# Performance work log

Measured on AMD Instinct MI355X. Metric: run time of the kernel, lower is better.

## Reference

```python
import jax, jax.numpy as jnp
import numpy as np

B, S_ENC, S_DEC = 4, 2048, 1024
ENC_DIM, DEC_DIM, H = 1024, 1024, 16
CROSS_DIM = max(ENC_DIM, DEC_DIM)
HEAD_DIM_DEC = DEC_DIM // H
SCALE = HEAD_DIM_DEC ** 0.5  # module divides by dec_scaling only


def _linear_params(key, d_in, d_out):
    kw, kb = jax.random.split(key)
    bound = 1.0 / np.sqrt(d_in)
    W = jax.random.uniform(kw, (d_in, d_out), jnp.float32, -bound, bound)
    b = jax.random.uniform(kb, (d_out,), jnp.float32, -bound, bound)
    return W, b


def setup_inputs() -> dict:
    key = jax.random.key(0)
    ks = jax.random.split(key, 7)
    enc = jax.random.normal(ks[0], (B, S_ENC, ENC_DIM), jnp.float32)
    dec = jax.random.normal(ks[1], (B, S_DEC, DEC_DIM), jnp.float32)
    enc_mask = jax.random.uniform(ks[2], (B, 1, 1, S_ENC)) < 0.1
    q_w, q_b = _linear_params(ks[3], DEC_DIM, CROSS_DIM)
    k_w, k_b = _linear_params(ks[4], ENC_DIM, CROSS_DIM)
    v_w, v_b = _linear_params(ks[5], ENC_DIM, DEC_DIM)
    o_w, o_b = _linear_params(ks[6], DEC_DIM, DEC_DIM)
    return {"enc": enc, "enc_mask": enc_mask, "dec": dec,
            "q_w": q_w, "q_b": q_b, "k_w": k_w, "k_b": k_b,
            "v_w": v_w, "v_b": v_b, "o_w": o_w, "o_b": o_b}


def _split_heads(x):
    b, s, d = x.shape
    return x.reshape(b, s, H, d // H).transpose(0, 2, 1, 3)  # [b,h,s,hd]


def reference(enc, enc_mask, dec, q_w, q_b, k_w, k_b, v_w, v_b, o_w, o_b):
    q = _split_heads(dec @ q_w + q_b)   # [B,H,Sq,cross_hd]
    k = _split_heads(enc @ k_w + k_b)   # [B,H,Sk,cross_hd]
    v = _split_heads(enc @ v_w + v_b)   # [B,H,Sk,dec_hd]
    logits = jnp.einsum('bhqd,bhkd->bhqk', q, k) / SCALE
    logits = jnp.where(enc_mask, -jnp.inf, logits)
    a = jax.nn.softmax(logits, axis=-1)
    x = jnp.einsum('bhqk,bhkd->bhqd', a, v)          # [B,H,Sq,dec_hd]
    x = x.transpose(0, 2, 1, 3).reshape(x.shape[0], x.shape[2], -1)  # [B,Sq,DEC_DIM]
    return x @ o_w + o_b
```

## Files before the change

kernel.cpp:

```cpp
#include <hip/hip_runtime.h>
#include <hip/hip_bf16.h>
#include <cstdint>

#define BB   4
#define SENC 2048
#define SDEC 1024
#define DM   1024
#define NH   16
#define HD   64

using short8 = __attribute__((ext_vector_type(8))) short;
using f32x4  = __attribute__((ext_vector_type(4))) float;

__device__ inline unsigned short f2bf(float f) {
    return (unsigned short)((__builtin_bit_cast(unsigned int, f) + 0x8000u) >> 16);
}
__device__ inline unsigned int pk2bf(float a, float b) {
    return ((__builtin_bit_cast(unsigned int, a) + 0x8000u) >> 16) |
           ((__builtin_bit_cast(unsigned int, b) + 0x8000u) & 0xffff0000u);
}

__device__ inline float fexp2(float x) {
#if __has_builtin(__builtin_amdgcn_exp2f)
    return __builtin_amdgcn_exp2f(x);
#else
    return exp2f(x);
#endif
}

#if __has_builtin(__builtin_amdgcn_global_load_lds)
#define HAS_GLL 1
#endif

__device__ inline void stage16(const void* g, void* l) {
#ifdef HAS_GLL
    typedef __attribute__((address_space(1))) const unsigned int guint;
    typedef __attribute__((address_space(3))) unsigned int luint;
    __builtin_amdgcn_global_load_lds((guint*)g, (luint*)l, 16, 0, 0);
#else
    *(short8*)l = *(const short8*)g;
#endif
}

__global__ __launch_bounds__(256) void prep_kernel(
    const float* __restrict__ dec, const float* __restrict__ enc,
    unsigned short* __restrict__ actb,
    const float* __restrict__ qw, const float* __restrict__ kw,
    const float* __restrict__ vw, const float* __restrict__ ow,
    unsigned short* __restrict__ qwt, unsigned short* __restrict__ kvwt,
    unsigned short* __restrict__ owt) {
    __shared__ float t[64][65];
    const int id = blockIdx.x, tid = threadIdx.x;
    if (id < 12288) {
        const int nd = BB * SDEC * DM;
        int i = (id * 256 + tid) * 4;
        const float* src = (i < nd) ? (dec + i) : (enc + (i - nd));
        float4 v = *(const float4*)src;
        ushort4 o;
        o.x = f2bf(v.x); o.y = f2bf(v.y); o.z = f2bf(v.z); o.w = f2bf(v.w);
        *(ushort4*)(actb + i) = o;
        return;
    }
    const int id2 = id - 12288;
    const int z = id2 >> 8, ky = (id2 >> 4) & 15, nx = id2 & 15;
    const float* src; unsigned short* dst;
    switch (z) {
        case 0:  src = qw; dst = qwt; break;
        case 1:  src = kw; dst = kvwt; break;
        case 2:  src = vw; dst = kvwt + (size_t)64 * 16384; break;
        default: src = ow; dst = owt; break;
    }
    const int k0 = ky * 64, n0 = nx * 64;
    #pragma unroll
    for (int it = 0; it < 16; ++it) {
        int e = it * 256 + tid, r = e >> 6, c = e & 63;
        t[r][c] = src[(size_t)(k0 + r) * DM + n0 + c];
    }
    __syncthreads();
    #pragma unroll
    for (int it = 0; it < 16; ++it) {
        int e = it * 256 + tid, r = e >> 6, c = e & 63;
        size_t off = (size_t)((n0 + r) >> 4) * 16384 + (size_t)((k0 + c) >> 3) * 128
                   + ((r & 15) << 3) + (c & 7);
        dst[off] = f2bf(t[c][r]);
    }
}

#define FENCE() asm volatile("" ::: "memory")
#define BARRIER() do { FENCE(); __builtin_amdgcn_s_barrier(); FENCE(); } while (0)

#define STAGE_TILE(kt, bufi) do { \
    stage16(Ab + (kt) * 64,          &As[bufi][tid * 8]); \
    stage16(Ab + 65536 + (kt) * 64,  &As[bufi][4096 + tid * 8]); \
    stage16(Ab + 131072 + (kt) * 64, &As[bufi][8192 + tid * 8]); \
    stage16(Ab + 196608 + (kt) * 64, &As[bufi][12288 + tid * 8]); \
} while (0)

#define LOADB(dst, kt) do { \
    dst[0][0] = *(const short8*)&Bbase[(kt) * 1024]; \
    dst[0][1] = *(const short8*)&Bbase[(kt) * 1024 + 512]; \
    dst[1][0] = *(const short8*)&Bbase[16384 + (kt) * 1024]; \
    dst[1][1] = *(const short8*)&Bbase[16384 + (kt) * 1024 + 512]; \
    dst[2][0] = *(const short8*)&Bbase[32768 + (kt) * 1024]; \
    dst[2][1] = *(const short8*)&Bbase[32768 + (kt) * 1024 + 512]; \
    dst[3][0] = *(const short8*)&Bbase[49152 + (kt) * 1024]; \
    dst[3][1] = *(const short8*)&Bbase[49152 + (kt) * 1024 + 512]; \
} while (0)

#define MFMA8(ii, a0, a1) do { \
    acc[ii][0] = __builtin_amdgcn_mfma_f32_16x16x32_bf16(a0, bcur[0][0], acc[ii][0], 0, 0, 0); \
    acc[ii][1] = __builtin_amdgcn_mfma_f32_16x16x32_bf16(a0, bcur[1][0], acc[ii][1], 0, 0, 0); \
    acc[ii][2] = __builtin_amdgcn_mfma_f32_16x16x32_bf16(a0, bcur[2][0], acc[ii][2], 0, 0, 0); \
    acc[ii][3] = __builtin_amdgcn_mfma_f32_16x16x32_bf16(a0, bcur[3][0], acc[ii][3], 0, 0, 0); \
    acc[ii][0] = __builtin_amdgcn_mfma_f32_16x16x32_bf16(a1, bcur[0][1], acc[ii][0], 0, 0, 0); \
    acc[ii][1] = __builtin_amdgcn_mfma_f32_16x16x32_bf16(a1, bcur[1][1], acc[ii][1], 0, 0, 0); \
    acc[ii][2] = __builtin_amdgcn_mfma_f32_16x16x32_bf16(a1, bcur[2][1], acc[ii][2], 0, 0, 0); \
    acc[ii][3] = __builtin_amdgcn_mfma_f32_16x16x32_bf16(a1, bcur[3][1], acc[ii][3], 0, 0, 0); \
} while (0)

__global__ __launch_bounds__(512, 2) void gemm_qkv_kernel(
    const unsigned short* __restrict__ encb, const unsigned short* __restrict__ decb,
    const unsigned short* __restrict__ kvwt, const unsigned short* __restrict__ qwt,
    const float* __restrict__ q_b, const float* __restrict__ k_b, const float* __restrict__ v_b,
    unsigned short* __restrict__ Qb, unsigned short* __restrict__ Kb,
    unsigned short* __restrict__ Vtb) {
    __shared__ __align__(16) unsigned short As[2][256 * 64];
    const int id = blockIdx.x;
    const bool isKV = id < 512;
    const unsigned short *A, *Bw;
    int m0, n0;
    if (isKV) {
        const int x = id & 7, w = id >> 3;
        A = encb; Bw = kvwt;
        m0 = (x * 4 + (w >> 4)) * 256;
        n0 = (w & 15) * 128;
    } else {
        const int i2 = id - 512, x = i2 & 7, w = i2 >> 3;
        A = decb; Bw = qwt;
        m0 = (x * 2 + (w >> 3)) * 256;
        n0 = (w & 7) * 128;
    }
    const int tid = threadIdx.x;
    const int wave = tid >> 6, lane = tid & 63, quad = lane >> 4, l16 = lane & 15;
    const int wr = wave >> 1, wc = wave & 1;
    f32x4 acc[4][4] = {};

    const int srow = tid >> 3;
    const int ksrc = ((tid ^ srow) & 7) * 8;
    const unsigned short* Ab = A + (size_t)(m0 + srow) * 1024 + ksrc;

    const unsigned short* Bbase = Bw + (size_t)((n0 >> 4) + wc * 4) * 16384 + quad * 128 + l16 * 8;
    short8 bcur[4][2], bnxt[4][2];

    const int rbase = (wr * 64 + l16) * 128;
    const int rswz = (l16 & 7) << 4;
    const int rk0 = (quad * 16) ^ rswz;
    const int rk1 = (64 + quad * 16) ^ rswz;

    STAGE_TILE(0, 0);
    FENCE();
    LOADB(bcur, 0);
    FENCE();
    STAGE_TILE(1, 1);
    FENCE();
    asm volatile("s_waitcnt vmcnt(12)" ::: "memory");
    __builtin_amdgcn_s_barrier();
    FENCE();

    #pragma unroll
    for (int kt = 0; kt <= 14; ++kt) {
        const char* ap = (const char*)&As[kt & 1][0] + rbase;
        short8 a00 = *(const short8*)(ap + rk0);
        short8 a01 = *(const short8*)(ap + rk1);
        short8 a10 = *(const short8*)(ap + 2048 + rk0);
        short8 a11 = *(const short8*)(ap + 2048 + rk1);
        if (kt >= 1) {
            STAGE_TILE(kt + 1, (kt & 1) ^ 1);
            FENCE();
        }
        LOADB(bnxt, kt + 1);
        FENCE();
        __builtin_amdgcn_s_barrier();
        FENCE();
        __builtin_amdgcn_s_setprio(1);
        MFMA8(0, a00, a01);
        MFMA8(1, a10, a11);
        __builtin_amdgcn_s_setprio(0);
        BARRIER();
        short8 a20 = *(const short8*)(ap + 4096 + rk0);
        short8 a21 = *(const short8*)(ap + 4096 + rk1);
        short8 a30 = *(const short8*)(ap + 6144 + rk0);
        short8 a31 = *(const short8*)(ap + 6144 + rk1);
        FENCE();
        __builtin_amdgcn_s_barrier();
        FENCE();
        __builtin_amdgcn_s_setprio(1);
        MFMA8(2, a20, a21);
        MFMA8(3, a30, a31);
        __builtin_amdgcn_s_setprio(0);
        asm volatile("s_waitcnt vmcnt(8)" ::: "memory");
        __builtin_amdgcn_s_barrier();
        FENCE();
        bcur[0][0] = bnxt[0][0]; bcur[0][1] = bnxt[0][1];
        bcur[1][0] = bnxt[1][0]; bcur[1][1] = bnxt[1][1];
        bcur[2][0] = bnxt[2][0]; bcur[2][1] = bnxt[2][1];
        bcur[3][0] = bnxt[3][0]; bcur[3][1] = bnxt[3][1];
    }
    {
        const char* ap = (const char*)&As[1][0] + rbase;
        short8 a00 = *(const short8*)(ap + rk0);
        short8 a01 = *(const short8*)(ap + rk1);
        short8 a10 = *(const short8*)(ap + 2048 + rk0);
        short8 a11 = *(const short8*)(ap + 2048 + rk1);
        __builtin_amdgcn_s_setprio(1);
        MFMA8(0, a00, a01);
        MFMA8(1, a10, a11);
        __builtin_amdgcn_s_setprio(0);
        short8 a20 = *(const short8*)(ap + 4096 + rk0);
        short8 a21 = *(const short8*)(ap + 4096 + rk1);
        short8 a30 = *(const short8*)(ap + 6144 + rk0);
        short8 a31 = *(const short8*)(ap + 6144 + rk1);
        __builtin_amdgcn_s_setprio(1);
        MFMA8(2, a20, a21);
        MFMA8(3, a30, a31);
        __builtin_amdgcn_s_setprio(0);
    }

    #pragma unroll
    for (int i = 0; i < 4; ++i) {
        #pragma unroll
        for (int j = 0; j < 4; ++j) {
            const int gc = n0 + wc * 64 + j * 16 + l16;
            const int gr0 = m0 + wr * 64 + i * 16 + quad * 4;
            if (!isKV) {
                const float bv = q_b[gc];
                const int h = gc >> 6, d = gc & 63;
                #pragma unroll
                for (int rr = 0; rr < 4; ++rr) {
                    int gr = gr0 + rr, b = gr >> 10, sq = gr & 1023;
                    float v = (acc[i][j][rr] + bv) * 0.18033688011112042f;
                    Qb[(((size_t)(b * NH + h) * SDEC + sq) << 6) + d] = f2bf(v);
                }
            } else if (gc < 1024) {
                const float bv = k_b[gc];
                const int h = gc >> 6, d = gc & 63;
                #pragma unroll
                for (int rr = 0; rr < 4; ++rr) {
                    int gr = gr0 + rr, b = gr >> 11, sk = gr & 2047;
                    size_t off = (size_t)(b * NH + h) * 131072 + (size_t)(sk >> 4) * 1024
                               + ((d >> 3) << 7) + ((sk & 15) << 3) + (d & 7);
                    Kb[off] = f2bf(acc[i][j][rr] + bv);
                }
            } else {
                const int gc2 = gc & 1023;
                const float bv = v_b[gc2];
                const int h = gc2 >> 6, d = gc2 & 63;
                const int b = gr0 >> 11, sk0 = gr0 & 2047;
                size_t off = (size_t)(b * NH + h) * 131072 + (size_t)(d >> 4) * 32768
                           + (size_t)(sk0 >> 3) * 128 + ((d & 15) << 3) + (sk0 & 7);
                uint2 pk;
                pk.x = pk2bf(acc[i][j][0] + bv, acc[i][j][1] + bv);
                pk.y = pk2bf(acc[i][j][2] + bv, acc[i][j][3] + bv);
                *(uint2*)&Vtb[off] = pk;
            }
        }
    }
}

__global__ __launch_bounds__(256) void gemm_o_kernel(const unsigned short* __restrict__ A,
                                                     const unsigned short* __restrict__ Bw,
                                                     const float* __restrict__ bias,
                                                     float* __restrict__ Cout) {
    __shared__ __align__(16) unsigned short As[2][64 * 32];
    const int id = blockIdx.x, x = id & 7, w = id >> 3;
    const int m0 = (x * 8 + (w >> 3)) * 64, n0 = (w & 7) * 128;
    const int tid = threadIdx.x;
    const int wave = tid >> 6, lane = tid & 63, quad = lane >> 4, l16 = lane & 15;
    const int r16 = lane >> 2, c8 = (lane & 3) * 8;
    f32x4 acc[4][2] = {};
    const unsigned short* Bbase = Bw + (size_t)((n0 >> 4) + wave * 2) * 16384 + quad * 128 + l16 * 8;
    short8 bcur[2], bnxt[2];
    #pragma unroll
    for (int j = 0; j < 2; ++j) bcur[j] = *(const short8*)&Bbase[j * 16384];
    {
        const int rowA = wave * 16 + r16;
        stage16(&A[(size_t)(m0 + rowA) * DM + c8], &As[0][rowA * 32 + c8]);
    }
    for (int it = 0; it < 32; ++it) {
        const int bf = it & 1;
        __syncthreads();
        if (it < 31) {
            const int kb2 = (it + 1) * 32, nb = bf ^ 1;
            const int rowA = wave * 16 + r16;
            stage16(&A[(size_t)(m0 + rowA) * DM + kb2 + c8], &As[nb][rowA * 32 + c8]);
            #pragma unroll
            for (int j = 0; j < 2; ++j) bnxt[j] = *(const short8*)&Bbase[j * 16384 + kb2 * 16];
        }
        short8 af[4];
        #pragma unroll
        for (int i = 0; i < 4; ++i) af[i] = *(const short8*)&As[bf][(i * 16 + l16) * 32 + quad * 8];
        #pragma unroll
        for (int i = 0; i < 4; ++i)
            #pragma unroll
            for (int j = 0; j < 2; ++j)
                acc[i][j] = __builtin_amdgcn_mfma_f32_16x16x32_bf16(af[i], bcur[j], acc[i][j], 0, 0, 0);
        #pragma unroll
        for (int j = 0; j < 2; ++j) bcur[j] = bnxt[j];
    }
    #pragma unroll
    for (int i = 0; i < 4; ++i)
        #pragma unroll
        for (int j = 0; j < 2; ++j) {
            const int gc = n0 + wave * 32 + j * 16 + l16;
            const float bv = bias[gc];
            #pragma unroll
            for (int rr = 0; rr < 4; ++rr) {
                const int gr = m0 + i * 16 + quad * 4 + rr;
                Cout[(size_t)gr * DM + gc] = acc[i][j][rr] + bv;
            }
        }
}

__global__ __launch_bounds__(256) void attn_kernel(const unsigned short* __restrict__ Qb,
                                                   const unsigned short* __restrict__ Kb,
                                                   const unsigned short* __restrict__ Vtb,
                                                   const int* __restrict__ mask,
                                                   unsigned short* __restrict__ Xb) {
    __shared__ __align__(16) unsigned short Ps[4][16 * 72];
    const int id = blockIdx.x, x = id & 7, r = id >> 3;
    const int bh = x * 8 + (r & 7), qt = r >> 3;
    const int b = bh >> 4, h = bh & 15;
    const int q0 = qt * 128;
    const int tid = threadIdx.x, wave = tid >> 6, lane = tid & 63;
    const int quad = lane >> 4, l16 = lane & 15;
    const int lo = quad * 128 + l16 * 8;

    const unsigned short* Kfp = Kb + (size_t)bh * 131072;
    const unsigned short* Vfp = Vtb + (size_t)bh * 131072;
    const int* mp = mask + (size_t)b * SENC;

    short8 qf[2][2];
    {
        const unsigned short* Qp = Qb + ((size_t)bh * SDEC + q0 + wave * 32) * HD;
        #pragma unroll
        for (int g = 0; g < 2; ++g) {
            qf[g][0] = *(const short8*)&Qp[(g * 16 + l16) * HD + quad * 8];
            qf[g][1] = *(const short8*)&Qp[(g * 16 + l16) * HD + 32 + quad * 8];
        }
    }

    float lsum[2] = {0.f, 0.f};
    f32x4 o[2][4] = {};

    for (int kb = 0; kb < SENC; kb += 64) {
        short8 kA0[4], kA1[4], vB0[4], vB1[4];
        const unsigned short* kt = Kfp + (size_t)(kb >> 4) * 1024 + lo;
        const unsigned short* vt = Vfp + (size_t)(kb >> 3) * 128 + lo;
        #pragma unroll
        for (int j = 0; j < 4; ++j) {
            kA0[j] = *(const short8*)&kt[j * 1024];
            kA1[j] = *(const short8*)&kt[j * 1024 + 512];
            vB0[j] = *(const short8*)&vt[j * 32768];
            vB1[j] = *(const short8*)&vt[j * 32768 + 512];
        }
        int4 mi[4];
        #pragma unroll
        for (int j = 0; j < 4; ++j) mi[j] = *(const int4*)&mp[kb + j * 16 + quad * 4];
        #pragma unroll
        for (int g = 0; g < 2; ++g) {
            f32x4 st[4];
            #pragma unroll
            for (int j = 0; j < 4; ++j) {
                f32x4 z = {0.f, 0.f, 0.f, 0.f};
                z = __builtin_amdgcn_mfma_f32_16x16x32_bf16(kA0[j], qf[g][0], z, 0, 0, 0);
                st[j] = __builtin_amdgcn_mfma_f32_16x16x32_bf16(kA1[j], qf[g][1], z, 0, 0, 0);
            }
            #pragma unroll
            for (int j = 0; j < 4; ++j) {
                float p0 = mi[j].x ? 0.f : fexp2(st[j][0]);
                float p1 = mi[j].y ? 0.f : fexp2(st[j][1]);
                float p2 = mi[j].z ? 0.f : fexp2(st[j][2]);
                float p3 = mi[j].w ? 0.f : fexp2(st[j][3]);
                lsum[g] += (p0 + p1) + (p2 + p3);
                uint2 pkv;
                pkv.x = pk2bf(p0, p1);
                pkv.y = pk2bf(p2, p3);
                *(uint2*)&Ps[wave][l16 * 72 + j * 16 + quad * 4] = pkv;
            }
            asm volatile("s_waitcnt lgkmcnt(0)" ::: "memory");
            short8 pA0 = *(const short8*)&Ps[wave][l16 * 72 + quad * 8];
            short8 pA1 = *(const short8*)&Ps[wave][l16 * 72 + 32 + quad * 8];
            #pragma unroll
            for (int dj = 0; dj < 4; ++dj) {
                o[g][dj] = __builtin_amdgcn_mfma_f32_16x16x32_bf16(pA0, vB0[dj], o[g][dj], 0, 0, 0);
                o[g][dj] = __builtin_amdgcn_mfma_f32_16x16x32_bf16(pA1, vB1[dj], o[g][dj], 0, 0, 0);
            }
        }
    }
    #pragma unroll
    for (int g = 0; g < 2; ++g) {
        float lg = lsum[g];
        lg += __shfl_xor(lg, 16);
        lg += __shfl_xor(lg, 32);
        #pragma unroll
        for (int rr = 0; rr < 4; ++rr) {
            float iv = 1.0f / __shfl(lg, quad * 4 + rr, 64);
            int sq = q0 + wave * 32 + g * 16 + quad * 4 + rr;
            #pragma unroll
            for (int dj = 0; dj < 4; ++dj)
                Xb[((size_t)(b * SDEC) + sq) * DM + h * HD + dj * 16 + l16] = f2bf(o[g][dj][rr] * iv);
        }
    }
}

extern "C" void kernel_launch(void* const* d_in, const int* in_sizes, int n_in,
                              void* d_out, int out_size, void* d_ws, size_t ws_size,
                              hipStream_t stream) {
    const float* enc   = (const float*)d_in[0];
    const int*   emask = (const int*)d_in[1];
    const float* dec   = (const float*)d_in[2];
    const float* q_w   = (const float*)d_in[3];
    const float* q_b   = (const float*)d_in[4];
    const float* k_w   = (const float*)d_in[5];
    const float* k_b   = (const float*)d_in[6];
    const float* v_w   = (const float*)d_in[7];
    const float* v_b   = (const float*)d_in[8];
    const float* o_w   = (const float*)d_in[9];
    const float* o_b   = (const float*)d_in[10];
    float* out = (float*)d_out;

    char* ws = (char*)d_ws;
    unsigned short* decb = (unsigned short*)ws; ws += (size_t)4096 * 1024 * 2;
    unsigned short* encb = (unsigned short*)ws; ws += (size_t)8192 * 1024 * 2;
    unsigned short* qwt  = (unsigned short*)ws; ws += (size_t)1024 * 1024 * 2;
    unsigned short* kvwt = (unsigned short*)ws; ws += (size_t)2048 * 1024 * 2;
    unsigned short* owt  = (unsigned short*)ws; ws += (size_t)1024 * 1024 * 2;
    unsigned short* Qb   = (unsigned short*)ws; ws += (size_t)BB * NH * SDEC * HD * 2;
    unsigned short* Kb   = (unsigned short*)ws; ws += (size_t)BB * NH * SENC * HD * 2;
    unsigned short* Vtb  = (unsigned short*)ws; ws += (size_t)BB * NH * HD * SENC * 2;
    unsigned short* Xb   = (unsigned short*)ws; ws += (size_t)4096 * 1024 * 2;

    prep_kernel<<<13312, 256, 0, stream>>>(dec, enc, decb, q_w, k_w, v_w, o_w, qwt, kvwt, owt);
    gemm_qkv_kernel<<<640, 512, 0, stream>>>(encb, decb, kvwt, qwt, q_b, k_b, v_b, Qb, Kb, Vtb);
    attn_kernel<<<512, 256, 0, stream>>>(Qb, Kb, Vtb, emask, Xb);
    gemm_o_kernel<<<512, 256, 0, stream>>>(Xb, owt, o_b, out);
}
```

Measured before the change: 272.3 us.

## Stage B weights through LDS with triple-buffered A/B pipeline in QKV GEMM

The QKV projection GEMM now loads weight tiles into shared memory alongside A tiles, instead of having each wave fetch B fragments straight from global memory into registers. It moves from a double buffer to a triple buffer with a prefetch distance of two tiles, and splits each tile's staging across the two MFMA phases. The goal is to hide more global latency and to drop the duplicate B global reads made by waves that share a column. In exchange, LDS use rises to about 144KB per block, which may break the two-blocks-per-CU launch bound and lower occupancy, and there are extra LDS reads for B.

```diff
diff --git a/kernel.cpp b/kernel.cpp
--- a/kernel.cpp
+++ b/kernel.cpp
@@ -89,33 +89,34 @@
 #define FENCE() asm volatile("" ::: "memory")
 #define BARRIER() do { FENCE(); __builtin_amdgcn_s_barrier(); FENCE(); } while (0)
 
-#define STAGE_TILE(kt, bufi) do { \
-    stage16(Ab + (kt) * 64,          &As[bufi][tid * 8]); \
-    stage16(Ab + 65536 + (kt) * 64,  &As[bufi][4096 + tid * 8]); \
-    stage16(Ab + 131072 + (kt) * 64, &As[bufi][8192 + tid * 8]); \
-    stage16(Ab + 196608 + (kt) * 64, &As[bufi][12288 + tid * 8]); \
+#define SP0(kt, sb) do { \
+    stage16(Ab + (kt) * 64,          &As[sb][tid * 8]); \
+    stage16(Ab + 65536 + (kt) * 64,  &As[sb][4096 + tid * 8]); \
+    stage16(Bg0 + (kt) * 1024,       &Bs[sb][tid * 8]); \
 } while (0)
-
-#define LOADB(dst, kt) do { \
-    dst[0][0] = *(const short8*)&Bbase[(kt) * 1024]; \
-    dst[0][1] = *(const short8*)&Bbase[(kt) * 1024 + 512]; \
-    dst[1][0] = *(const short8*)&Bbase[16384 + (kt) * 1024]; \
-    dst[1][1] = *(const short8*)&Bbase[16384 + (kt) * 1024 + 512]; \
-    dst[2][0] = *(const short8*)&Bbase[32768 + (kt) * 1024]; \
-    dst[2][1] = *(const short8*)&Bbase[32768 + (kt) * 1024 + 512]; \
-    dst[3][0] = *(const short8*)&Bbase[49152 + (kt) * 1024]; \
-    dst[3][1] = *(const short8*)&Bbase[49152 + (kt) * 1024 + 512]; \
+#define SP1(kt, sb) do { \
+    stage16(Ab + 131072 + (kt) * 64, &As[sb][8192 + tid * 8]); \
+    stage16(Ab + 196608 + (kt) * 64, &As[sb][12288 + tid * 8]); \
+    stage16(Bg1 + (kt) * 1024,       &Bs[sb][4096 + tid * 8]); \
 } while (0)
 
-#define MFMA8(ii, a0, a1) do { \
-    acc[ii][0] = __builtin_amdgcn_mfma_f32_16x16x32_bf16(a0, bcur[0][0], acc[ii][0], 0, 0, 0); \
-    acc[ii][1] = __builtin_amdgcn_mfma_f32_16x16x32_bf16(a0, bcur[1][0], acc[ii][1], 0, 0, 0); \
-    acc[ii][2] = __builtin_amdgcn_mfma_f32_16x16x32_bf16(a0, bcur[2][0], acc[ii][2], 0, 0, 0); \
-    acc[ii][3] = __builtin_amdgcn_mfma_f32_16x16x32_bf16(a0, bcur[3][0], acc[ii][3], 0, 0, 0); \
-    acc[ii][0] = __builtin_amdgcn_mfma_f32_16x16x32_bf16(a1, bcur[0][1], acc[ii][0], 0, 0, 0); \
-    acc[ii][1] = __builtin_amdgcn_mfma_f32_16x16x32_bf16(a1, bcur[1][1], acc[ii][1], 0, 0, 0); \
-    acc[ii][2] = __builtin_amdgcn_mfma_f32_16x16x32_bf16(a1, bcur[2][1], acc[ii][2], 0, 0, 0); \
-    acc[ii][3] = __builtin_amdgcn_mfma_f32_16x16x32_bf16(a1, bcur[3][1], acc[ii][3], 0, 0, 0); \
+#define MM(i, ak0, ak1) do { \
+    acc[i][0] = __builtin_amdgcn_mfma_f32_16x16x32_bf16(ak0, bb[0][0], acc[i][0], 0, 0, 0); \
+    acc[i][1] = __builtin_amdgcn_mfma_f32_16x16x32_bf16(ak0, bb[1][0], acc[i][1], 0, 0, 0); \
+    acc[i][2] = __builtin_amdgcn_mfma_f32_16x16x32_bf16(ak0, bb[2][0], acc[i][2], 0, 0, 0); \
+    acc[i][3] = __builtin_amdgcn_mfma_f32_16x16x32_bf16(ak0, bb[3][0], acc[i][3], 0, 0, 0); \
+    acc[i][0] = __builtin_amdgcn_mfma_f32_16x16x32_bf16(ak1, bb[0][1], acc[i][0], 0, 0, 0); \
+    acc[i][1] = __builtin_amdgcn_mfma_f32_16x16x32_bf16(ak1, bb[1][1], acc[i][1], 0, 0, 0); \
+    acc[i][2] = __builtin_amdgcn_mfma_f32_16x16x32_bf16(ak1, bb[2][1], acc[i][2], 0, 0, 0); \
+    acc[i][3] = __builtin_amdgcn_mfma_f32_16x16x32_bf16(ak1, bb[3][1], acc[i][3], 0, 0, 0); \
+} while (0)
+
+#define LOADBB(ct) do { \
+    const unsigned short* bp = &Bs[ct][bfrag]; \
+    bb[0][0] = *(const short8*)&bp[0];    bb[0][1] = *(const short8*)&bp[512]; \
+    bb[1][0] = *(const short8*)&bp[1024]; bb[1][1] = *(const short8*)&bp[1536]; \
+    bb[2][0] = *(const short8*)&bp[2048]; bb[2][1] = *(const short8*)&bp[2560]; \
+    bb[3][0] = *(const short8*)&bp[3072]; bb[3][1] = *(const short8*)&bp[3584]; \
 } while (0)
 
 __global__ __launch_bounds__(512, 2) void gemm_qkv_kernel(
@@ -124,7 +125,8 @@
     const float* __restrict__ q_b, const float* __restrict__ k_b, const float* __restrict__ v_b,
     unsigned short* __restrict__ Qb, unsigned short* __restrict__ Kb,
     unsigned short* __restrict__ Vtb) {
-    __shared__ __align__(16) unsigned short As[2][256 * 64];
+    __shared__ __align__(16) unsigned short As[3][16384];
+    __shared__ __align__(16) unsigned short Bs[3][8192];
     const int id = blockIdx.x;
     const bool isKV = id < 512;
     const unsigned short *A, *Bw;
@@ -148,81 +150,99 @@
     const int srow = tid >> 3;
     const int ksrc = ((tid ^ srow) & 7) * 8;
     const unsigned short* Ab = A + (size_t)(m0 + srow) * 1024 + ksrc;
-
-    const unsigned short* Bbase = Bw + (size_t)((n0 >> 4) + wc * 4) * 16384 + quad * 128 + l16 * 8;
-    short8 bcur[4][2], bnxt[4][2];
+    const unsigned short* Bg0 = Bw + (size_t)((n0 >> 4) + (tid >> 7)) * 16384 + (tid & 127) * 8;
+    const unsigned short* Bg1 = Bg0 + (size_t)4 * 16384;
 
     const int rbase = (wr * 64 + l16) * 128;
     const int rswz = (l16 & 7) << 4;
     const int rk0 = (quad * 16) ^ rswz;
     const int rk1 = (64 + quad * 16) ^ rswz;
-
-    STAGE_TILE(0, 0);
+    const int bfrag = wc * 4096 + quad * 128 + l16 * 8;
+
+    SP0(0, 0); SP1(0, 0);
+    SP0(1, 1); SP1(1, 1);
     FENCE();
-    LOADB(bcur, 0);
-    FENCE();
-    STAGE_TILE(1, 1);
-    FENCE();
-    asm volatile("s_waitcnt vmcnt(12)" ::: "memory");
+    asm volatile("s_waitcnt vmcnt(6)" ::: "memory");
     __builtin_amdgcn_s_barrier();
     FENCE();
 
-    #pragma unroll
-    for (int kt = 0; kt <= 14; ++kt) {
-        const char* ap = (const char*)&As[kt & 1][0] + rbase;
+    int ct = 0, st = 2;
+    for (int kt = 0; kt < 14; ++kt) {
+        const char* ap = (const char*)&As[ct][0] + rbase;
+        short8 bb[4][2];
+        LOADBB(ct);
         short8 a00 = *(const short8*)(ap + rk0);
         short8 a01 = *(const short8*)(ap + rk1);
         short8 a10 = *(const short8*)(ap + 2048 + rk0);
         short8 a11 = *(const short8*)(ap + 2048 + rk1);
-        if (kt >= 1) {
-            STAGE_TILE(kt + 1, (kt & 1) ^ 1);
-            FENCE();
-        }
-        LOADB(bnxt, kt + 1);
+        SP0(kt + 2, st);
         FENCE();
         __builtin_amdgcn_s_barrier();
         FENCE();
         __builtin_amdgcn_s_setprio(1);
-        MFMA8(0, a00, a01);
-        MFMA8(1, a10, a11);
+        MM(0, a00, a01);
+        MM(1, a10, a11);
         __builtin_amdgcn_s_setprio(0);
         BARRIER();
         short8 a20 = *(const short8*)(ap + 4096 + rk0);
         short8 a21 = *(const short8*)(ap + 4096 + rk1);
         short8 a30 = *(const short8*)(ap + 6144 + rk0);
         short8 a31 = *(const short8*)(ap + 6144 + rk1);
-        FENCE();
+        SP1(kt + 2, st);
+        FENCE();
+        asm volatile("s_waitcnt vmcnt(6)" ::: "memory");
         __builtin_amdgcn_s_barrier();
         FENCE();
         __builtin_amdgcn_s_setprio(1);
-        MFMA8(2, a20, a21);
-        MFMA8(3, a30, a31);
+        MM(2, a20, a21);
+        MM(3, a30, a31);
         __builtin_amdgcn_s_setprio(0);
-        asm volatile("s_waitcnt vmcnt(8)" ::: "memory");
-        __builtin_amdgcn_s_barrier();
-        FENCE();
-        bcur[0][0] = bnxt[0][0]; bcur[0][1] = bnxt[0][1];
-        bcur[1][0] = bnxt[1][0]; bcur[1][1] = bnxt[1][1];
-        bcur[2][0] = bnxt[2][0]; bcur[2][1] = bnxt[2][1];
-        bcur[3][0] = bnxt[3][0]; bcur[3][1] = bnxt[3][1];
+        BARRIER();
+        ct = (ct == 2) ? 0 : ct + 1;
+        st = (st == 2) ? 0 : st + 1;
     }
     {
-        const char* ap = (const char*)&As[1][0] + rbase;
+        const char* ap = (const char*)&As[2][0] + rbase;
+        short8 bb[4][2];
+        LOADBB(2);
         short8 a00 = *(const short8*)(ap + rk0);
         short8 a01 = *(const short8*)(ap + rk1);
         short8 a10 = *(const short8*)(ap + 2048 + rk0);
         short8 a11 = *(const short8*)(ap + 2048 + rk1);
         __builtin_amdgcn_s_setprio(1);
-        MFMA8(0, a00, a01);
-        MFMA8(1, a10, a11);
+        MM(0, a00, a01);
+        MM(1, a10, a11);
         __builtin_amdgcn_s_setprio(0);
         short8 a20 = *(const short8*)(ap + 4096 + rk0);
         short8 a21 = *(const short8*)(ap + 4096 + rk1);
         short8 a30 = *(const short8*)(ap + 6144 + rk0);
         short8 a31 = *(const short8*)(ap + 6144 + rk1);
         __builtin_amdgcn_s_setprio(1);
-        MFMA8(2, a20, a21);
-        MFMA8(3, a30, a31);
+        MM(2, a20, a21);
+        MM(3, a30, a31);
+        __builtin_amdgcn_s_setprio(0);
+        FENCE();
+        asm volatile("s_waitcnt vmcnt(0)" ::: "memory");
+        __builtin_amdgcn_s_barrier();
+        FENCE();
+    }
+    {
+        const char* ap = (const char*)&As[0][0] + rbase;
+        short8 bb[4][2];
+        LOADBB(0);
+        short8 a00 = *(const short8*)(ap + rk0);
+        short8 a01 = *(const short8*)(ap + rk1);
+        short8 a10 = *(const short8*)(ap + 2048 + rk0);
+        short8 a11 = *(const short8*)(ap + 2048 + rk1);
+        short8 a20 = *(const short8*)(ap + 4096 + rk0);
+        short8 a21 = *(const short8*)(ap + 4096 + rk1);
+        short8 a30 = *(const short8*)(ap + 6144 + rk0);
+        short8 a31 = *(const short8*)(ap + 6144 + rk1);
+        __builtin_amdgcn_s_setprio(1);
+        MM(0, a00, a01);
+        MM(1, a10, a11);
+        MM(2, a20, a21);
+        MM(3, a30, a31);
         __builtin_amdgcn_s_setprio(0);
     }
 
```

After: 261.5 us. 1.04x faster.
